# Optimization experiments

Hardware: AMD Instinct MI355X
Metric: run time of the kernel (lower is better)

## Reference

```python
import jax, jax.numpy as jnp
import numpy as np

B, S, E, H = 2, 2048, 1024, 16
D = E // H  # head_dim = 64

def setup_inputs() -> dict:
    key = jax.random.key(0)
    ks = jax.random.split(key, 11)
    s = 1.0 / np.sqrt(E)
    inp = {
        'query': jax.random.normal(ks[0], (B, S, E), jnp.float32),
        'key':   jax.random.normal(ks[1], (B, S, E), jnp.float32),
        'value': jax.random.normal(ks[2], (B, S, E), jnp.float32),
        'Wq': jax.random.uniform(ks[3], (E, E), jnp.float32, -s, s),
        'bq': jax.random.uniform(ks[4], (E,), jnp.float32, -s, s),
        'Wk': jax.random.uniform(ks[5], (E, E), jnp.float32, -s, s),
        'bk': jax.random.uniform(ks[6], (E,), jnp.float32, -s, s),
        'Wv': jax.random.uniform(ks[7], (E, E), jnp.float32, -s, s),
        'bv': jax.random.uniform(ks[8], (E,), jnp.float32, -s, s),
        'Wo': jax.random.uniform(ks[9], (E, E), jnp.float32, -s, s),
        'bo': jax.random.uniform(ks[10], (E,), jnp.float32, -s, s),
    }
    return inp

def reference(query, key, value, Wq, bq, Wk, bk, Wv, bv, Wo, bo):
    # project and split heads: [B,S,E] -> [B,H,S,D]
    def proj(x, W, b):
        y = jnp.einsum('bse,fe->bsf', x, W) + b  # torch Linear: x @ W.T + b
        return y.reshape(B, S, H, D).transpose(0, 2, 1, 3)
    q = proj(query, Wq, bq)
    k = proj(key, Wk, bk)
    v = proj(value, Wv, bv)
    scores = jnp.einsum('bhqd,bhkd->bhqk', q, k) / jnp.sqrt(jnp.float32(D))
    attn = jax.nn.softmax(scores, axis=-1)
    out = jnp.einsum('bhqk,bhkd->bhqd', attn, v)  # [B,H,S,D]
    out = out.transpose(0, 2, 1, 3).reshape(B, S, E)
    return jnp.einsum('bse,fe->bsf', out, Wo) + bo
```

## Files before the change

### kernel.cpp

```cpp
#include <hip/hip_runtime.h>

#define B_ 2
#define S_ 2048
#define E_ 1024
#define H_ 16
#define D_ 64
#define M_ (B_*S_)
#define K_ E_

typedef __attribute__((ext_vector_type(8))) short  short8;
typedef __attribute__((ext_vector_type(4))) float  f32x4;
typedef __attribute__((ext_vector_type(8))) unsigned short u16x8;
typedef __attribute__((ext_vector_type(4))) unsigned short u16x4;
typedef __attribute__((ext_vector_type(4))) unsigned int   u32x4;

#define QSCALE 0.18033688011112042f

#if __has_builtin(__builtin_amdgcn_exp2f)
#define EXP2F(x) __builtin_amdgcn_exp2f(x)
#else
#define EXP2F(x) exp2f(x)
#endif

__device__ __forceinline__ unsigned short f2bf(float f) {
    unsigned u = __float_as_uint(f);
    u += 0x7fffu + ((u >> 16) & 1u);
    return (unsigned short)(u >> 16);
}

__device__ __forceinline__ void gl_lds16(const ushort* g, ushort* l) {
    __builtin_amdgcn_global_load_lds((const __attribute__((address_space(1))) void*)g,
                                     (__attribute__((address_space(3))) void*)l,
                                     16, 0, 0);
}

#define FL_SYNC(N) do {                                                   \
    asm volatile("s_waitcnt vmcnt(" #N ")" ::: "memory");                 \
    __builtin_amdgcn_s_barrier();                                         \
    asm volatile("" ::: "memory");                                        \
} while (0)

__global__ __launch_bounds__(256)
void cvt_all(const float* __restrict__ q, const float* __restrict__ k,
             const float* __restrict__ v, const float* __restrict__ wq,
             const float* __restrict__ wk, const float* __restrict__ wv,
             const float* __restrict__ wo, ushort* __restrict__ dst)
{
    const int bid = blockIdx.x;
    const float* src;
    size_t dof;
    int local;
    if (bid < 6144) {
        const int t = bid >> 11;
        src = (t == 0) ? q : (t == 1) ? k : v;
        dof = (size_t)t * 4194304u;
        local = bid & 2047;
    } else {
        const int r = bid - 6144;
        const int t = r >> 9;
        src = (t == 0) ? wq : (t == 1) ? wk : (t == 2) ? wv : wo;
        dof = 12582912u + (size_t)t * 1048576u;
        local = r & 511;
    }
    const size_t idx = (size_t)local * 2048 + threadIdx.x * 8;
    const float4 a = *(const float4*)(src + idx);
    const float4 b = *(const float4*)(src + idx + 4);
    u16x8 o;
    o[0] = f2bf(a.x); o[1] = f2bf(a.y); o[2] = f2bf(a.z); o[3] = f2bf(a.w);
    o[4] = f2bf(b.x); o[5] = f2bf(b.y); o[6] = f2bf(b.z); o[7] = f2bf(b.w);
    *(u16x8*)(dst + dof + idx) = o;
}

template<int SWAP>
__device__ __forceinline__ void gemm_core(const ushort* __restrict__ X,
                                          const ushort* __restrict__ W,
                                          int m0, int n0,
                                          f32x4 acc[4][4],
                                          ushort* Ast, ushort* Bst)
{
    const int tid  = threadIdx.x;
    const int lane = tid & 63;
    const int w    = tid >> 6;
    const int wm   = w & 1, wn = w >> 1;
    const int r0   = tid >> 2;
    const int c8   = (tid & 3) * 8;

    const f32x4 zero = {0.f, 0.f, 0.f, 0.f};
    #pragma unroll
    for (int mt = 0; mt < 4; ++mt)
        #pragma unroll
        for (int nt = 0; nt < 4; ++nt) acc[mt][nt] = zero;

    const int kb = (lane >> 4) * 8;

    for (int k0 = 0; k0 < K_; k0 += 32) {
        __syncthreads();
        const ushort* ga = X + (size_t)(m0 + r0) * K_ + k0 + c8;
        gl_lds16(ga, Ast + tid * 8);
        gl_lds16(ga + (size_t)64 * K_, Ast + 2048 + tid * 8);
        const ushort* gb = W + (size_t)(n0 + r0) * K_ + k0 + c8;
        gl_lds16(gb, Bst + tid * 8);
        gl_lds16(gb + (size_t)64 * K_, Bst + 2048 + tid * 8);
        __syncthreads();

        short8 af[4], bf[4];
        #pragma unroll
        for (int mt = 0; mt < 4; ++mt)
            af[mt] = *(const short8*)(Ast + (wm * 64 + mt * 16 + (lane & 15)) * 32 + kb);
        #pragma unroll
        for (int nt = 0; nt < 4; ++nt)
            bf[nt] = *(const short8*)(Bst + (wn * 64 + nt * 16 + (lane & 15)) * 32 + kb);
        #pragma unroll
        for (int mt = 0; mt < 4; ++mt)
            #pragma unroll
            for (int nt = 0; nt < 4; ++nt) {
                if (SWAP)
                    acc[mt][nt] = __builtin_amdgcn_mfma_f32_16x16x32_bf16(bf[nt], af[mt], acc[mt][nt], 0, 0, 0);
                else
                    acc[mt][nt] = __builtin_amdgcn_mfma_f32_16x16x32_bf16(af[mt], bf[nt], acc[mt][nt], 0, 0, 0);
            }
    }
}

__global__ __launch_bounds__(256)
void gemm_qkv(const ushort* __restrict__ Xq, const ushort* __restrict__ Xk,
              const ushort* __restrict__ Xv, const ushort* __restrict__ Wq,
              const ushort* __restrict__ Wk, const ushort* __restrict__ Wv,
              const float* __restrict__ bq, const float* __restrict__ bk,
              const float* __restrict__ bv, ushort* __restrict__ Qh,
              ushort* __restrict__ Kh, ushort* __restrict__ Vt)
{
    __shared__ ushort Ast[128 * 32];
    __shared__ ushort Bst[128 * 32];
    const int z = blockIdx.z;
    const ushort* X = (z == 0) ? Xq : (z == 1) ? Xk : Xv;
    const ushort* W = (z == 0) ? Wq : (z == 1) ? Wk : Wv;
    const float* bias = (z == 0) ? bq : (z == 1) ? bk : bv;
    ushort* dst = (z == 0) ? Qh : (z == 1) ? Kh : Vt;

    const int m0 = blockIdx.y * 128, n0 = blockIdx.x * 128;
    f32x4 acc[4][4];
    const int lane = threadIdx.x & 63, w = threadIdx.x >> 6;
    const int wm = w & 1, wn = w >> 1;
    const int l15 = lane & 15, quad = lane >> 4;

    if (z < 2) {
        gemm_core<1>(X, W, m0, n0, acc, Ast, Bst);
        const float qsc = (z == 0) ? QSCALE : 1.0f;
        #pragma unroll
        for (int nt = 0; nt < 4; ++nt) {
            const int nb = n0 + wn * 64 + nt * 16 + quad * 4;
            const int h = nb >> 6, d0 = nb & 63;
            const float4 b4 = *(const float4*)(bias + nb);
            const float bb4[4] = {b4.x, b4.y, b4.z, b4.w};
            #pragma unroll
            for (int mt = 0; mt < 4; ++mt) {
                const int tok = m0 + wm * 64 + mt * 16 + l15;
                const int b = tok >> 11, s = tok & (S_ - 1);
                u16x4 pk;
                #pragma unroll
                for (int r = 0; r < 4; ++r)
                    pk[r] = f2bf((acc[mt][nt][r] + bb4[r]) * qsc);
                *(u16x4*)&dst[(((size_t)(b * H_ + h) * S_) + s) * D_ + d0] = pk;
            }
        }
    } else {
        gemm_core<0>(X, W, m0, n0, acc, Ast, Bst);
        float bias4[4];
        #pragma unroll
        for (int nt = 0; nt < 4; ++nt)
            bias4[nt] = bias[n0 + wn * 64 + nt * 16 + l15];
        #pragma unroll
        for (int mt = 0; mt < 4; ++mt) {
            const int mrow0 = m0 + wm * 64 + mt * 16 + (quad * 4);
            const int b = mrow0 >> 11;
            const int s0 = mrow0 & (S_ - 1);
            #pragma unroll
            for (int nt = 0; nt < 4; ++nt) {
                const int n = n0 + wn * 64 + nt * 16 + l15;
                const int h = n >> 6, d = n & 63;
                u16x4 pk;
                #pragma unroll
                for (int r = 0; r < 4; ++r) pk[r] = f2bf(acc[mt][nt][r] + bias4[nt]);
                *(u16x4*)&Vt[(((size_t)(b * H_ + h) * D_) + d) * S_ + s0] = pk;
            }
        }
    }
}

__global__ __launch_bounds__(256)
void gemm_out(const ushort* __restrict__ X, const ushort* __restrict__ W,
              const float* __restrict__ bias, float* __restrict__ out)
{
    __shared__ ushort Ast[128 * 32];
    __shared__ ushort Bst[64 * 32];
    const int m0 = blockIdx.y * 128, n0 = blockIdx.x * 64;
    const int tid = threadIdx.x, lane = tid & 63, w = tid >> 6;
    const int wm = w & 1, wn = w >> 1;
    const int l15 = lane & 15, quad = lane >> 4;
    const int r0 = tid >> 2, c8 = (tid & 3) * 8;
    const int kb = quad * 8;

    const f32x4 zero = {0.f, 0.f, 0.f, 0.f};
    f32x4 acc[4][2];
    #pragma unroll
    for (int mt = 0; mt < 4; ++mt)
        #pragma unroll
        for (int nt = 0; nt < 2; ++nt) acc[mt][nt] = zero;

    for (int k0 = 0; k0 < K_; k0 += 32) {
        __syncthreads();
        const ushort* ga = X + (size_t)(m0 + r0) * K_ + k0 + c8;
        gl_lds16(ga, Ast + tid * 8);
        gl_lds16(ga + (size_t)64 * K_, Ast + 2048 + tid * 8);
        const ushort* gb = W + (size_t)(n0 + r0) * K_ + k0 + c8;
        gl_lds16(gb, Bst + tid * 8);
        __syncthreads();

        short8 af[4], bf[2];
        #pragma unroll
        for (int mt = 0; mt < 4; ++mt)
            af[mt] = *(const short8*)(Ast + (wm * 64 + mt * 16 + l15) * 32 + kb);
        #pragma unroll
        for (int nt = 0; nt < 2; ++nt)
            bf[nt] = *(const short8*)(Bst + (wn * 32 + nt * 16 + l15) * 32 + kb);
        #pragma unroll
        for (int mt = 0; mt < 4; ++mt)
            #pragma unroll
            for (int nt = 0; nt < 2; ++nt)
                acc[mt][nt] = __builtin_amdgcn_mfma_f32_16x16x32_bf16(af[mt], bf[nt], acc[mt][nt], 0, 0, 0);
    }

    float bias2[2];
    #pragma unroll
    for (int nt = 0; nt < 2; ++nt)
        bias2[nt] = bias[n0 + wn * 32 + nt * 16 + l15];

    #pragma unroll
    for (int mt = 0; mt < 4; ++mt) {
        const int mrow0 = m0 + wm * 64 + mt * 16 + quad * 4;
        #pragma unroll
        for (int nt = 0; nt < 2; ++nt) {
            const int n = n0 + wn * 32 + nt * 16 + l15;
            #pragma unroll
            for (int r = 0; r < 4; ++r)
                out[(size_t)(mrow0 + r) * E_ + n] = acc[mt][nt][r] + bias2[nt];
        }
    }
}

#define NTILE (S_ / 64)

__device__ __forceinline__ void flash_stage(const ushort* __restrict__ Kg,
                                            const ushort* __restrict__ Vg,
                                            size_t qk_off, size_t vt_off,
                                            ushort* sh, int j,
                                            int row0, int gcol0, int row1, int gcol1,
                                            int chunk0, int chunk1, int lane)
{
    ushort* sb = sh + 4096 + (j & 3) * 8192;
    const int j0n = j * 64;
    gl_lds16(Kg + qk_off + (size_t)(j0n + row0) * D_ + gcol0 * 8, sb + chunk0 * 512 + lane * 8);
    gl_lds16(Vg + vt_off + (size_t)row0 * S_ + j0n + gcol0 * 8, sb + 4096 + chunk0 * 512 + lane * 8);
    gl_lds16(Kg + qk_off + (size_t)(j0n + row1) * D_ + gcol1 * 8, sb + chunk1 * 512 + lane * 8);
    gl_lds16(Vg + vt_off + (size_t)row1 * S_ + j0n + gcol1 * 8, sb + 4096 + chunk1 * 512 + lane * 8);
}

__device__ __forceinline__ void flash_qk(const ushort* Kb, const ushort* Vb,
                                         const short8* qr0, const short8* qr1,
                                         int krow, int l15, int quad, int gidx,
                                         float* lsum, uint2* pout, uint2* vv)
{
    const short8 ka0 = *(const short8*)&Kb[krow + ((quad ^ (l15 & 7)) * 8)];
    const short8 ka1 = *(const short8*)&Kb[krow + (((4 + quad) ^ (l15 & 7)) * 8)];
    #pragma unroll
    for (int nt = 0; nt < 4; ++nt)
        vv[nt] = *(const uint2*)&Vb[(nt * 16 + l15) * 64 + gidx * 8 + (quad & 1) * 4];
    const f32x4 zero = {0.f, 0.f, 0.f, 0.f};
    #pragma unroll
    for (int g = 0; g < 4; ++g) {
        f32x4 t;
        t = __builtin_amdgcn_mfma_f32_16x16x32_bf16(ka0, qr0[g], zero, 0, 0, 0);
        t = __builtin_amdgcn_mfma_f32_16x16x32_bf16(ka1, qr1[g], t, 0, 0, 0);
        const float p0 = EXP2F(t[0]), p1 = EXP2F(t[1]);
        const float p2 = EXP2F(t[2]), p3 = EXP2F(t[3]);
        lsum[g] += (p0 + p1) + (p2 + p3);
        const unsigned a0 = __float_as_uint(p0) + 0x8000u;
        const unsigned a1 = __float_as_uint(p1) + 0x8000u;
        const unsigned a2 = __float_as_uint(p2) + 0x8000u;
        const unsigned a3 = __float_as_uint(p3) + 0x8000u;
        pout[g].x = (a1 & 0xffff0000u) | (a0 >> 16);
        pout[g].y = (a3 & 0xffff0000u) | (a2 >> 16);
    }
}

__device__ __forceinline__ void flash_pv(const uint2* paLo, const uint2* paHi,
                                         const uint2* vvA, const uint2* vvB,
                                         f32x4 o[4][4])
{
    short8 pa8[4];
    #pragma unroll
    for (int g = 0; g < 4; ++g) {
        u32x4 pk;
        pk[0] = paLo[g].x; pk[1] = paLo[g].y;
        pk[2] = paHi[g].x; pk[3] = paHi[g].y;
        pa8[g] = __builtin_bit_cast(short8, pk);
    }
    #pragma unroll
    for (int nt = 0; nt < 4; ++nt) {
        u32x4 vk;
        vk[0] = vvA[nt].x; vk[1] = vvA[nt].y;
        vk[2] = vvB[nt].x; vk[3] = vvB[nt].y;
        const short8 vb8 = __builtin_bit_cast(short8, vk);
        #pragma unroll
        for (int g = 0; g < 4; ++g)
            o[g][nt] = __builtin_amdgcn_mfma_f32_16x16x32_bf16(pa8[g], vb8, o[g][nt], 0, 0, 0);
    }
}

__global__ __launch_bounds__(256, 2)
void flash_mfma(const ushort* __restrict__ Qg, const ushort* __restrict__ Kg,
                const ushort* __restrict__ Vg, ushort* __restrict__ AO)
{
    __shared__ ushort sh[36864];
    ushort* Qs = sh;

    const int tid = threadIdx.x, lane = tid & 63, w = tid >> 6;
    const int l15 = lane & 15, quad = lane >> 4;
    const int q0 = blockIdx.x * 64, h = blockIdx.y, b = blockIdx.z;
    const size_t qk_off = (size_t)(b * H_ + h) * S_ * D_;
    const size_t vt_off = (size_t)(b * H_ + h) * D_ * S_;

    const int chunk0 = w, chunk1 = w + 4;
    const int row0 = chunk0 * 8 + (lane >> 3);
    const int row1 = chunk1 * 8 + (lane >> 3);
    const int gcol0 = (lane & 7) ^ (row0 & 7);
    const int gcol1 = (lane & 7) ^ (row1 & 7);

    gl_lds16(Qg + qk_off + (size_t)(q0 + row0) * D_ + gcol0 * 8, Qs + chunk0 * 512 + lane * 8);
    gl_lds16(Qg + qk_off + (size_t)(q0 + row1) * D_ + gcol1 * 8, Qs + chunk1 * 512 + lane * 8);
    flash_stage(Kg, Vg, qk_off, vt_off, sh, 0, row0, gcol0, row1, gcol1, chunk0, chunk1, lane);
    flash_stage(Kg, Vg, qk_off, vt_off, sh, 1, row0, gcol0, row1, gcol1, chunk0, chunk1, lane);
    flash_stage(Kg, Vg, qk_off, vt_off, sh, 2, row0, gcol0, row1, gcol1, chunk0, chunk1, lane);

    FL_SYNC(12);

    short8 qr0[4], qr1[4];
    #pragma unroll
    for (int g = 0; g < 4; ++g) {
        qr0[g] = *(const short8*)&Qs[(g * 16 + l15) * 64 + ((quad ^ (l15 & 7)) * 8)];
        qr1[g] = *(const short8*)&Qs[(g * 16 + l15) * 64 + (((4 + quad) ^ (l15 & 7)) * 8)];
    }

    const f32x4 zero = {0.f, 0.f, 0.f, 0.f};
    f32x4 o[4][4];
    #pragma unroll
    for (int g = 0; g < 4; ++g)
        #pragma unroll
        for (int nt = 0; nt < 4; ++nt) o[g][nt] = zero;
    float lsum[4] = {0.f, 0.f, 0.f, 0.f};

    const int krow = (w * 16 + l15) * 64;
    const int gidx = (2 * w + (quad >> 1)) ^ (l15 & 7);

    uint2 vvA[4], vvB[4], paLo[4], paHi[4];

    for (int p = 0; p < 15; ++p) {
        const int jA = 2 * p;
        FL_SYNC(8);
        flash_stage(Kg, Vg, qk_off, vt_off, sh, jA + 3,
                    row0, gcol0, row1, gcol1, chunk0, chunk1, lane);
        {
            const ushort* KbA = sh + 4096 + (jA & 3) * 8192;
            flash_qk(KbA, KbA + 4096, qr0, qr1, krow, l15, quad, gidx, lsum, paLo, vvA);
        }
        FL_SYNC(8);
        if (jA + 4 < NTILE)
            flash_stage(Kg, Vg, qk_off, vt_off, sh, jA + 4,
                        row0, gcol0, row1, gcol1, chunk0, chunk1, lane);
        {
            const ushort* KbB = sh + 4096 + ((jA + 1) & 3) * 8192;
            flash_qk(KbB, KbB + 4096, qr0, qr1, krow, l15, quad, gidx, lsum, paHi, vvB);
        }
        flash_pv(paLo, paHi, vvA, vvB, o);
    }

    FL_SYNC(4);
    {
        const ushort* KbA = sh + 4096 + (30 & 3) * 8192;
        flash_qk(KbA, KbA + 4096, qr0, qr1, krow, l15, quad, gidx, lsum, paLo, vvA);
    }
    FL_SYNC(0);
    {
        const ushort* KbB = sh + 4096 + (31 & 3) * 8192;
        flash_qk(KbB, KbB + 4096, qr0, qr1, krow, l15, quad, gidx, lsum, paHi, vvB);
    }
    flash_pv(paLo, paHi, vvA, vvB, o);

    #pragma unroll
    for (int g = 0; g < 4; ++g) {
        lsum[g] += __shfl_xor(lsum[g], 16);
        lsum[g] += __shfl_xor(lsum[g], 32);
    }
    __syncthreads();
    float* fb = (float*)sh;
    #pragma unroll
    for (int g = 0; g < 4; ++g) {
        if (w != g) {
            #pragma unroll
            for (int nt = 0; nt < 4; ++nt)
                #pragma unroll
                for (int r = 0; r < 4; ++r)
                    fb[w * 1024 + (nt * 4 + r) * 64 + lane] = o[g][nt][r];
            if (quad == 0) fb[4096 + w * 64 + l15] = lsum[g];
        }
        __syncthreads();
        if (w == g) {
            #pragma unroll
            for (int ws = 0; ws < 4; ++ws) {
                if (ws == g) continue;
                #pragma unroll
                for (int nt = 0; nt < 4; ++nt)
                    #pragma unroll
                    for (int r = 0; r < 4; ++r)
                        o[g][nt][r] += fb[ws * 1024 + (nt * 4 + r) * 64 + lane];
                lsum[g] += fb[4096 + ws * 64 + l15];
            }
        }
        __syncthreads();
    }

    #pragma unroll
    for (int g = 0; g < 4; ++g) {
        if (w == g) {
            const float inv = 1.0f / lsum[g];
            float invr[4];
            #pragma unroll
            for (int r = 0; r < 4; ++r)
                invr[r] = __shfl(inv, (lane & 0x30) | (quad * 4 + r));
            #pragma unroll
            for (int nt = 0; nt < 4; ++nt) {
                const int e = h * 64 + nt * 16 + l15;
                #pragma unroll
                for (int r = 0; r < 4; ++r) {
                    const int s = q0 + g * 16 + quad * 4 + r;
                    AO[(size_t)(b * S_ + s) * E_ + e] = f2bf(o[g][nt][r] * invr[r]);
                }
            }
        }
    }
}

extern "C" void kernel_launch(void* const* d_in, const int* in_sizes, int n_in,
                              void* d_out, int out_size, void* d_ws, size_t ws_size,
                              hipStream_t stream) {
    const float* query = (const float*)d_in[0];
    const float* key   = (const float*)d_in[1];
    const float* value = (const float*)d_in[2];
    const float* Wq = (const float*)d_in[3];
    const float* bq = (const float*)d_in[4];
    const float* Wk = (const float*)d_in[5];
    const float* bk = (const float*)d_in[6];
    const float* Wv = (const float*)d_in[7];
    const float* bv = (const float*)d_in[8];
    const float* Wo = (const float*)d_in[9];
    const float* bo = (const float*)d_in[10];
    float* out = (float*)d_out;

    ushort* ws = (ushort*)d_ws;
    ushort* Xq  = ws;
    ushort* Xk  = ws + 4194304u;
    ushort* Xv  = ws + 8388608u;
    ushort* Wqb = ws + 12582912u;
    ushort* Wkb = ws + 13631488u;
    ushort* Wvb = ws + 14680064u;
    ushort* Wob = ws + 15728640u;
    ushort* Qh  = ws + 16777216u;
    ushort* Kh  = ws + 20971520u;
    ushort* Vt  = ws + 25165824u;
    ushort* AO  = ws + 29360128u;

    cvt_all<<<8192, 256, 0, stream>>>(query, key, value, Wq, Wk, Wv, Wo, ws);
    gemm_qkv<<<dim3(8, 32, 3), 256, 0, stream>>>(Xq, Xk, Xv, Wqb, Wkb, Wvb,
                                                 bq, bk, bv, Qh, Kh, Vt);
    flash_mfma<<<dim3(32, 16, 2), 256, 0, stream>>>(Qh, Kh, Vt, AO);
    gemm_out<<<dim3(16, 32), 256, 0, stream>>>(AO, Wob, bo, out);
}
```

Measured before the change: 231.7 us.

## Restructure QKV GEMM into 256x256 tiles with double-buffered swizzled LDS

Rewrites the QKV projection GEMM core to use 512-thread blocks computing 256x256 output tiles with a 64-wide K step. Global-to-LDS loads are double-buffered and issued two stages ahead, with an XOR swizzle on LDS columns to avoid bank conflicts. It also raises wave priority around the MFMA section. The aim is more data reuse per LDS load and overlap of loads with compute, but the grid shrinks to 192 blocks, fewer than the CU count, and the 128KB LDS footprint limits occupancy.

```diff
diff --git a/kernel.cpp b/kernel.cpp
--- a/kernel.cpp
+++ b/kernel.cpp
@@ -36,6 +36,12 @@
 
 #define FL_SYNC(N) do {                                                   \
     asm volatile("s_waitcnt vmcnt(" #N ")" ::: "memory");                 \
+    __builtin_amdgcn_s_barrier();                                         \
+    asm volatile("" ::: "memory");                                        \
+} while (0)
+
+#define WAITL0_BAR() do {                                                 \
+    asm volatile("s_waitcnt lgkmcnt(0)" ::: "memory");                    \
     __builtin_amdgcn_s_barrier();                                         \
     asm volatile("" ::: "memory");                                        \
 } while (0)
@@ -72,57 +78,92 @@
 }
 
 template<int SWAP>
-__device__ __forceinline__ void gemm_core(const ushort* __restrict__ X,
-                                          const ushort* __restrict__ W,
-                                          int m0, int n0,
-                                          f32x4 acc[4][4],
-                                          ushort* Ast, ushort* Bst)
+__device__ __forceinline__ void qkv_core(const ushort* __restrict__ X,
+                                         const ushort* __restrict__ W,
+                                         int m0, int n0,
+                                         f32x4 acc[8][4], ushort* sh)
 {
     const int tid  = threadIdx.x;
     const int lane = tid & 63;
     const int w    = tid >> 6;
-    const int wm   = w & 1, wn = w >> 1;
-    const int r0   = tid >> 2;
-    const int c8   = (tid & 3) * 8;
+    const int wm   = w & 1;
+    const int wn   = w >> 1;
+    const int l15  = lane & 15, quad = lane >> 4;
+
+    const int srow = lane >> 3, schunk = lane & 7;
+    const int scol = (schunk ^ srow) * 8;
+    const ushort* pa[4]; const ushort* pb[4]; int loff[4];
+    #pragma unroll
+    for (int i = 0; i < 4; ++i) {
+        const int row = (w * 4 + i) * 8 + srow;
+        pa[i] = X + (size_t)(m0 + row) * K_ + scol;
+        pb[i] = W + (size_t)(n0 + row) * K_ + scol;
+        loff[i] = (w * 4 + i) * 512 + lane * 8;
+    }
 
     const f32x4 zero = {0.f, 0.f, 0.f, 0.f};
     #pragma unroll
-    for (int mt = 0; mt < 4; ++mt)
+    for (int mt = 0; mt < 8; ++mt)
         #pragma unroll
         for (int nt = 0; nt < 4; ++nt) acc[mt][nt] = zero;
 
-    const int kb = (lane >> 4) * 8;
-
-    for (int k0 = 0; k0 < K_; k0 += 32) {
-        __syncthreads();
-        const ushort* ga = X + (size_t)(m0 + r0) * K_ + k0 + c8;
-        gl_lds16(ga, Ast + tid * 8);
-        gl_lds16(ga + (size_t)64 * K_, Ast + 2048 + tid * 8);
-        const ushort* gb = W + (size_t)(n0 + r0) * K_ + k0 + c8;
-        gl_lds16(gb, Bst + tid * 8);
-        gl_lds16(gb + (size_t)64 * K_, Bst + 2048 + tid * 8);
-        __syncthreads();
-
-        short8 af[4], bf[4];
-        #pragma unroll
-        for (int mt = 0; mt < 4; ++mt)
-            af[mt] = *(const short8*)(Ast + (wm * 64 + mt * 16 + (lane & 15)) * 32 + kb);
-        #pragma unroll
-        for (int nt = 0; nt < 4; ++nt)
-            bf[nt] = *(const short8*)(Bst + (wn * 64 + nt * 16 + (lane & 15)) * 32 + kb);
-        #pragma unroll
-        for (int mt = 0; mt < 4; ++mt)
+    #pragma unroll
+    for (int i = 0; i < 4; ++i) {
+        gl_lds16(pa[i],      sh + loff[i]);
+        gl_lds16(pb[i],      sh + 16384 + loff[i]);
+    }
+    #pragma unroll
+    for (int i = 0; i < 4; ++i) {
+        gl_lds16(pa[i] + 64, sh + 32768 + loff[i]);
+        gl_lds16(pb[i] + 64, sh + 32768 + 16384 + loff[i]);
+    }
+
+    const int arow = wm * 128 + l15;
+    const int brow = wn * 64 + l15;
+
+    for (int t = 0; t < 16; ++t) {
+        ushort* curA = sh + (t & 1) * 32768;
+        ushort* curB = curA + 16384;
+
+        if (t < 15) { FL_SYNC(8); } else { FL_SYNC(0); }
+
+        __builtin_amdgcn_s_setprio(1);
+        #pragma unroll
+        for (int kc = 0; kc < 2; ++kc) {
+            short8 bf[4];
             #pragma unroll
             for (int nt = 0; nt < 4; ++nt) {
-                if (SWAP)
-                    acc[mt][nt] = __builtin_amdgcn_mfma_f32_16x16x32_bf16(bf[nt], af[mt], acc[mt][nt], 0, 0, 0);
-                else
-                    acc[mt][nt] = __builtin_amdgcn_mfma_f32_16x16x32_bf16(af[mt], bf[nt], acc[mt][nt], 0, 0, 0);
-            }
-    }
-}
-
-__global__ __launch_bounds__(256)
+                const int r = brow + nt * 16;
+                bf[nt] = *(const short8*)(curB + r * 64 + (((kc * 4 + quad) ^ (r & 7)) * 8));
+            }
+            #pragma unroll
+            for (int mt = 0; mt < 8; ++mt) {
+                const int r = arow + mt * 16;
+                const short8 af = *(const short8*)(curA + r * 64 + (((kc * 4 + quad) ^ (r & 7)) * 8));
+                #pragma unroll
+                for (int nt = 0; nt < 4; ++nt) {
+                    if (SWAP)
+                        acc[mt][nt] = __builtin_amdgcn_mfma_f32_16x16x32_bf16(bf[nt], af, acc[mt][nt], 0, 0, 0);
+                    else
+                        acc[mt][nt] = __builtin_amdgcn_mfma_f32_16x16x32_bf16(af, bf[nt], acc[mt][nt], 0, 0, 0);
+                }
+            }
+        }
+        __builtin_amdgcn_s_setprio(0);
+
+        if (t + 2 < 16) {
+            WAITL0_BAR();
+            const int k0 = (t + 2) * 64;
+            #pragma unroll
+            for (int i = 0; i < 4; ++i) {
+                gl_lds16(pa[i] + k0, curA + loff[i]);
+                gl_lds16(pb[i] + k0, curB + loff[i]);
+            }
+        }
+    }
+}
+
+__global__ __launch_bounds__(512, 2)
 void gemm_qkv(const ushort* __restrict__ Xq, const ushort* __restrict__ Xk,
               const ushort* __restrict__ Xv, const ushort* __restrict__ Wq,
               const ushort* __restrict__ Wk, const ushort* __restrict__ Wv,
@@ -130,22 +171,21 @@
               const float* __restrict__ bv, ushort* __restrict__ Qh,
               ushort* __restrict__ Kh, ushort* __restrict__ Vt)
 {
-    __shared__ ushort Ast[128 * 32];
-    __shared__ ushort Bst[128 * 32];
+    __shared__ ushort sh[65536];
     const int z = blockIdx.z;
     const ushort* X = (z == 0) ? Xq : (z == 1) ? Xk : Xv;
     const ushort* W = (z == 0) ? Wq : (z == 1) ? Wk : Wv;
     const float* bias = (z == 0) ? bq : (z == 1) ? bk : bv;
     ushort* dst = (z == 0) ? Qh : (z == 1) ? Kh : Vt;
 
-    const int m0 = blockIdx.y * 128, n0 = blockIdx.x * 128;
-    f32x4 acc[4][4];
+    const int m0 = blockIdx.y * 256, n0 = blockIdx.x * 256;
+    f32x4 acc[8][4];
     const int lane = threadIdx.x & 63, w = threadIdx.x >> 6;
     const int wm = w & 1, wn = w >> 1;
     const int l15 = lane & 15, quad = lane >> 4;
 
     if (z < 2) {
-        gemm_core<1>(X, W, m0, n0, acc, Ast, Bst);
+        qkv_core<1>(X, W, m0, n0, acc, sh);
         const float qsc = (z == 0) ? QSCALE : 1.0f;
         #pragma unroll
         for (int nt = 0; nt < 4; ++nt) {
@@ -154,8 +194,8 @@
             const float4 b4 = *(const float4*)(bias + nb);
             const float bb4[4] = {b4.x, b4.y, b4.z, b4.w};
             #pragma unroll
-            for (int mt = 0; mt < 4; ++mt) {
-                const int tok = m0 + wm * 64 + mt * 16 + l15;
+            for (int mt = 0; mt < 8; ++mt) {
+                const int tok = m0 + wm * 128 + mt * 16 + l15;
                 const int b = tok >> 11, s = tok & (S_ - 1);
                 u16x4 pk;
                 #pragma unroll
@@ -165,14 +205,14 @@
             }
         }
     } else {
-        gemm_core<0>(X, W, m0, n0, acc, Ast, Bst);
+        qkv_core<0>(X, W, m0, n0, acc, sh);
         float bias4[4];
         #pragma unroll
         for (int nt = 0; nt < 4; ++nt)
             bias4[nt] = bias[n0 + wn * 64 + nt * 16 + l15];
         #pragma unroll
-        for (int mt = 0; mt < 4; ++mt) {
-            const int mrow0 = m0 + wm * 64 + mt * 16 + (quad * 4);
+        for (int mt = 0; mt < 8; ++mt) {
+            const int mrow0 = m0 + wm * 128 + mt * 16 + (quad * 4);
             const int b = mrow0 >> 11;
             const int s0 = mrow0 & (S_ - 1);
             #pragma unroll
@@ -481,7 +521,7 @@
     ushort* AO  = ws + 29360128u;
 
     cvt_all<<<8192, 256, 0, stream>>>(query, key, value, Wq, Wk, Wv, Wo, ws);
-    gemm_qkv<<<dim3(8, 32, 3), 256, 0, stream>>>(Xq, Xk, Xv, Wqb, Wkb, Wvb,
+    gemm_qkv<<<dim3(4, 16, 3), 512, 0, stream>>>(Xq, Xk, Xv, Wqb, Wkb, Wvb,
                                                  bq, bk, bv, Qh, Kh, Vt);
     flash_mfma<<<dim3(32, 16, 2), 256, 0, stream>>>(Qh, Kh, Vt, AO);
     gemm_out<<<dim3(16, 32), 256, 0, stream>>>(AO, Wob, bo, out);
```

Result: no change. 228.7 us (-1.3%).
